# Kernel optimization log

Measured on AMD Instinct MI355X. Metric: run time of the kernel, lower is better.

Reference implementation:

```python
import jax, jax.numpy as jnp
import numpy as np

D_MODEL = 1024
NUM_HEAD = 16
BATCH = 2
SEQ = 2048
NEG_INF = -1e9  # matches masked_fill value in the original


def setup_inputs() -> dict:
    key = jax.random.key(0)
    k1, k2, k3, k4, k5 = jax.random.split(key, 5)
    scale = 1.0 / np.sqrt(D_MODEL)
    return {
        "x": jax.random.normal(k1, (BATCH, SEQ, D_MODEL), dtype=jnp.float32),
        "q_weight": jax.random.normal(k2, (D_MODEL, D_MODEL), dtype=jnp.float32) * scale,
        "k_weight": jax.random.normal(k3, (D_MODEL, D_MODEL), dtype=jnp.float32) * scale,
        "v_weight": jax.random.normal(k4, (D_MODEL, D_MODEL), dtype=jnp.float32) * scale,
        "o_weight": jax.random.normal(k5, (D_MODEL, D_MODEL), dtype=jnp.float32) * scale,
    }


def reference(x, q_weight, k_weight, v_weight, o_weight):
    b, s, d = x.shape
    h = NUM_HEAD
    dh = d // h
    # projections: weight layout is (d_out, d_in)
    q = jnp.einsum('bsd,ed->bse', x, q_weight).reshape(b, s, h, dh).transpose(0, 2, 1, 3)
    k = jnp.einsum('bsd,ed->bse', x, k_weight).reshape(b, s, h, dh).transpose(0, 2, 1, 3)
    v = jnp.einsum('bsd,ed->bse', x, v_weight).reshape(b, s, h, dh).transpose(0, 2, 1, 3)
    scores = jnp.einsum('bhqd,bhkd->bhqk', q, k) / jnp.sqrt(jnp.asarray(dh, x.dtype))
    causal = jnp.triu(jnp.ones((s, s), dtype=bool), k=1)  # True above diagonal -> masked
    scores = jnp.where(causal, jnp.asarray(NEG_INF, x.dtype), scores)
    attn = jax.nn.softmax(scores, axis=-1)
    out = jnp.einsum('bhqk,bhkd->bhqd', attn, v)          # [b,h,s,dh]
    out = out.transpose(0, 2, 1, 3).reshape(b, s, d)       # merge heads
    return jnp.einsum('bse,de->bsd', out, o_weight)
```

## Files before the change

### kernel.cpp

```cpp
#include <hip/hip_runtime.h>

typedef short bhalf8 __attribute__((ext_vector_type(8)));
typedef float floatx4 __attribute__((ext_vector_type(4)));

#define D_MODEL 1024
#define SEQ     2048
#define BATCH   2
#define NHEAD   16
#define DH      64

#define GLDS(g, l) __builtin_amdgcn_global_load_lds( \
    (const __attribute__((address_space(1))) void*)(g), \
    (__attribute__((address_space(3))) void*)(l), 16, 0, 0)

static __device__ __forceinline__ short f2bf(float f) {
    unsigned u = __builtin_bit_cast(unsigned, f);
    u = (u + 0x7fffu + ((u >> 16) & 1u)) >> 16;
    return (short)u;
}
static __device__ __forceinline__ unsigned pack2(float a, float b) {
    return (unsigned)(unsigned short)f2bf(a) | ((unsigned)(unsigned short)f2bf(b) << 16);
}
static __device__ __forceinline__ unsigned cvt_pk_bf16(float lo, float hi) {
    unsigned r;
    asm("v_cvt_pk_bf16_f32 %0, %1, %2" : "=v"(r) : "v"(lo), "v"(hi));
    return r;
}

__global__ __launch_bounds__(256) void cast_x(const float* __restrict__ s,
                                              short* __restrict__ d) {
    int i = (blockIdx.x * 256 + threadIdx.x) * 8;
    float4 a = *(const float4*)(s + i);
    float4 b = *(const float4*)(s + i + 4);
    uint4 u = {pack2(a.x, a.y), pack2(a.z, a.w), pack2(b.x, b.y), pack2(b.z, b.w)};
    *(uint4*)(d + i) = u;
}

__global__ __launch_bounds__(256) void cast_w(const float* __restrict__ wq,
                                              const float* __restrict__ wk,
                                              const float* __restrict__ wv,
                                              const float* __restrict__ wo,
                                              short* __restrict__ dst) {
    const float* s = (blockIdx.y == 0) ? wq : (blockIdx.y == 1) ? wk
                   : (blockIdx.y == 2) ? wv : wo;
    size_t off = (size_t)blockIdx.y * (D_MODEL * D_MODEL);
    int i = (blockIdx.x * 256 + threadIdx.x) * 8;
    float4 a = *(const float4*)(s + i);
    float4 b = *(const float4*)(s + i + 4);
    uint4 u = {pack2(a.x, a.y), pack2(a.z, a.w), pack2(b.x, b.y), pack2(b.z, b.w)};
    *(uint4*)(dst + off + i) = u;
}

__global__ __launch_bounds__(256) void gemm_qkv(const short* __restrict__ A,
                                                const short* __restrict__ W,
                                                short* __restrict__ Qo,
                                                short* __restrict__ Ko,
                                                short* __restrict__ Vt) {
    __shared__ __align__(16) char pool[34816];
    short (*As)[64] = (short(*)[64])pool;
    short (*Bs)[64] = (short(*)[64])(pool + 16384);
    const int t    = threadIdx.x;
    const int wave = t >> 6, lane = t & 63, quad = lane >> 4, l16 = lane & 15;
    const int bm = blockIdx.x * 128, by = blockIdx.y, bn = by * 128;
    const int qm = (wave >> 1) * 64, qn = (wave & 1) * 64;

    const int lrow = lane >> 3, lcol = (lane & 7) * 8;
    const short* Ag = A + (size_t)(bm + wave * 32 + lrow) * 1024 + lcol;
    const short* Wg = W + (size_t)(bn + wave * 32 + lrow) * 1024 + lcol;
    short* Al = &As[wave * 32][0];
    short* Bl = &Bs[wave * 32][0];

    floatx4 acc[4][4];
#pragma unroll
    for (int i = 0; i < 4; ++i)
#pragma unroll
        for (int j = 0; j < 4; ++j) {
            floatx4 z = {0.f, 0.f, 0.f, 0.f};
            acc[i][j] = z;
        }

    for (int k0 = 0; k0 < 1024; k0 += 64) {
        __syncthreads();
#pragma unroll
        for (int j = 0; j < 4; ++j) {
            GLDS(Ag + k0 + (size_t)j * 8 * 1024, Al + j * 8 * 64);
            GLDS(Wg + k0 + (size_t)j * 8 * 1024, Bl + j * 8 * 64);
        }
        __syncthreads();
#pragma unroll
        for (int kk = 0; kk < 64; kk += 32) {
            bhalf8 af[4], bfr[4];
#pragma unroll
            for (int im = 0; im < 4; ++im)
                af[im] = *(const bhalf8*)&As[qm + im * 16 + l16][kk + quad * 8];
#pragma unroll
            for (int jn = 0; jn < 4; ++jn)
                bfr[jn] = *(const bhalf8*)&Bs[qn + jn * 16 + l16][kk + quad * 8];
#pragma unroll
            for (int im = 0; im < 4; ++im)
#pragma unroll
                for (int jn = 0; jn < 4; ++jn)
                    acc[im][jn] = __builtin_amdgcn_mfma_f32_16x16x32_bf16(
                        af[im], bfr[jn], acc[im][jn], 0, 0, 0);
        }
    }

    __syncthreads();
    short (*Ct)[136] = (short(*)[136])pool;
    const bool isV = (by >= 16);
#pragma unroll
    for (int im = 0; im < 4; ++im)
#pragma unroll
        for (int jn = 0; jn < 4; ++jn)
#pragma unroll
            for (int g = 0; g < 4; ++g) {
                const int ml = qm + im * 16 + quad * 4 + g;
                const int nl = qn + jn * 16 + l16;
                if (isV) Ct[nl][ml] = f2bf(acc[im][jn][g]);
                else     Ct[ml][nl] = f2bf(acc[im][jn][g]);
            }
    __syncthreads();

    short* outp;
    size_t rowbase, colbase, stride;
    if (by < 8)       { outp = Qo; rowbase = bm;                colbase = bn;        stride = 1024; }
    else if (by < 16) { outp = Ko; rowbase = bm;                colbase = bn - 1024; stride = 1024; }
    else              { outp = Vt; rowbase = (size_t)bn - 2048; colbase = bm;        stride = 4096; }
#pragma unroll
    for (int pass = 0; pass < 8; ++pass) {
        const int r = (t >> 4) + pass * 16;
        const int c = (t & 15) * 8;
        uint4 u = *(const uint4*)&Ct[r][c];
        *(uint4*)(outp + (rowbase + r) * stride + colbase + c) = u;
    }
}

__global__ __launch_bounds__(256) void gemm_o(const short* __restrict__ A,
                                              const short* __restrict__ W,
                                              float* __restrict__ C) {
    __shared__ __align__(16) char pool[34816];
    short (*As)[64] = (short(*)[64])pool;
    short (*Bs)[64] = (short(*)[64])(pool + 16384);
    const int t    = threadIdx.x;
    const int wave = t >> 6, lane = t & 63, quad = lane >> 4, l16 = lane & 15;
    const int bm = blockIdx.x * 128, bn = blockIdx.y * 64;
    const int qm = (wave >> 1) * 64, qn = (wave & 1) * 32;

    const int lrow = lane >> 3, lcol = (lane & 7) * 8;
    const short* Ag = A + (size_t)(bm + wave * 32 + lrow) * 1024 + lcol;
    const short* Wg = W + (size_t)(bn + wave * 16 + lrow) * 1024 + lcol;
    short* Al = &As[wave * 32][0];
    short* Bl = &Bs[wave * 16][0];

    floatx4 acc[4][2];
#pragma unroll
    for (int i = 0; i < 4; ++i)
#pragma unroll
        for (int j = 0; j < 2; ++j) {
            floatx4 z = {0.f, 0.f, 0.f, 0.f};
            acc[i][j] = z;
        }

    for (int k0 = 0; k0 < 1024; k0 += 64) {
        __syncthreads();
#pragma unroll
        for (int j = 0; j < 4; ++j)
            GLDS(Ag + k0 + (size_t)j * 8 * 1024, Al + j * 8 * 64);
#pragma unroll
        for (int j = 0; j < 2; ++j)
            GLDS(Wg + k0 + (size_t)j * 8 * 1024, Bl + j * 8 * 64);
        __syncthreads();
#pragma unroll
        for (int kk = 0; kk < 64; kk += 32) {
            bhalf8 af[4], bfr[2];
#pragma unroll
            for (int im = 0; im < 4; ++im)
                af[im] = *(const bhalf8*)&As[qm + im * 16 + l16][kk + quad * 8];
#pragma unroll
            for (int jn = 0; jn < 2; ++jn)
                bfr[jn] = *(const bhalf8*)&Bs[qn + jn * 16 + l16][kk + quad * 8];
#pragma unroll
            for (int im = 0; im < 4; ++im)
#pragma unroll
                for (int jn = 0; jn < 2; ++jn)
                    acc[im][jn] = __builtin_amdgcn_mfma_f32_16x16x32_bf16(
                        af[im], bfr[jn], acc[im][jn], 0, 0, 0);
        }
    }

    __syncthreads();
    float (*Ctf)[68] = (float(*)[68])pool;
#pragma unroll
    for (int im = 0; im < 4; ++im)
#pragma unroll
        for (int jn = 0; jn < 2; ++jn)
#pragma unroll
            for (int g = 0; g < 4; ++g)
                Ctf[qm + im * 16 + quad * 4 + g][qn + jn * 16 + l16] = acc[im][jn][g];
    __syncthreads();
#pragma unroll
    for (int pass = 0; pass < 8; ++pass) {
        const int r = (t >> 4) + pass * 16;
        const int c = (t & 15) * 4;
        float4 u = *(const float4*)&Ctf[r][c];
        *(float4*)(C + (size_t)(bm + r) * 1024 + bn + c) = u;
    }
}

#define LOADQ(qf, qwv) do {                                                   \
    _Pragma("unroll")                                                         \
    for (int im_ = 0; im_ < 2; ++im_) {                                       \
        const short* qr_ = Qbase + (size_t)((qwv) + im_ * 16 + l16) * 1024;   \
        qf[im_][0] = *(const bhalf8*)(qr_ + quad * 8);                        \
        qf[im_][1] = *(const bhalf8*)(qr_ + 32 + quad * 8);                   \
    } } while (0)

#define LOADK(dst, kk) do {                                                   \
    _Pragma("unroll")                                                         \
    for (int jn_ = 0; jn_ < 4; ++jn_) {                                       \
        const short* kr_ = Kbase + (size_t)((kk) + jn_ * 16 + l16) * 1024 + quad * 8; \
        dst[jn_][0] = *(const bhalf8*)(kr_);                                  \
        dst[jn_][1] = *(const bhalf8*)(kr_ + 32);                             \
    } } while (0)

#define LOADV(dst, kk) do {                                                   \
    _Pragma("unroll")                                                         \
    for (int nd_ = 0; nd_ < 4; ++nd_) {                                       \
        const short* vr_ = Vbase + (size_t)(nd_ * 16 + l16) * 4096 + (kk) + quad * 8; \
        dst[nd_][0] = *(const bhalf8*)(vr_);                                  \
        dst[nd_][1] = *(const bhalf8*)(vr_ + 32);                             \
    } } while (0)

#define ZERO_ACC() do {                                                       \
    _Pragma("unroll")                                                         \
    for (int im_ = 0; im_ < 2; ++im_) {                                       \
        _Pragma("unroll")                                                     \
        for (int g_ = 0; g_ < 4; ++g_) lsum[im_][g_] = 0.f;                   \
        _Pragma("unroll")                                                     \
        for (int nd_ = 0; nd_ < 4; ++nd_) {                                   \
            floatx4 z_ = {0.f, 0.f, 0.f, 0.f};                                \
            o[im_][nd_] = z_;                                                 \
        }                                                                     \
    } } while (0)

#define CHUNK(k0v, knv, qf, qwv) do {                                         \
    floatx4 s_[2][4];                                                         \
    _Pragma("unroll")                                                         \
    for (int im_ = 0; im_ < 2; ++im_)                                         \
        _Pragma("unroll")                                                     \
        for (int jn_ = 0; jn_ < 4; ++jn_) {                                   \
            floatx4 z_ = {0.f, 0.f, 0.f, 0.f};                                \
            z_ = __builtin_amdgcn_mfma_f32_16x16x32_bf16(qf[im_][0], kf[jn_][0], z_, 0, 0, 0); \
            z_ = __builtin_amdgcn_mfma_f32_16x16x32_bf16(qf[im_][1], kf[jn_][1], z_, 0, 0, 0); \
            s_[im_][jn_] = z_;                                                \
        }                                                                     \
    LOADK(kf, knv);                                \
    const bool partial_ = ((k0v) + 64 > (qwv));                               \
    _Pragma("unroll")                                                         \
    for (int im_ = 0; im_ < 2; ++im_)                                         \
        _Pragma("unroll")                                                     \
        for (int g_ = 0; g_ < 4; ++g_) {                                      \
            const int rr_ = im_ * 16 + quad * 4 + g_;                         \
            const int qrow_ = (qwv) + rr_;                                    \
            float e0_ = exp2f(s_[im_][0][g_] * KS - CB);                      \
            float e1_ = exp2f(s_[im_][1][g_] * KS - CB);                      \
            float e2_ = exp2f(s_[im_][2][g_] * KS - CB);                      \
            float e3_ = exp2f(s_[im_][3][g_] * KS - CB);                      \
            if (partial_) {                                                   \
                if ((k0v) + l16 > qrow_)      e0_ = 0.f;                      \
                if ((k0v) + 16 + l16 > qrow_) e1_ = 0.f;                      \
                if ((k0v) + 32 + l16 > qrow_) e2_ = 0.f;                      \
                if ((k0v) + 48 + l16 > qrow_) e3_ = 0.f;                      \
            }                                                                 \
            lsum[im_][g_] += (e0_ + e1_) + (e2_ + e3_);                       \
            unsigned r01_ = cvt_pk_bf16(e0_, e1_);                            \
            unsigned r23_ = cvt_pk_bf16(e2_, e3_);                            \
            Ps[wave][rr_][l16]      = (short)r01_;                            \
            Ps[wave][rr_][16 + l16] = (short)(r01_ >> 16);                    \
            Ps[wave][rr_][32 + l16] = (short)r23_;                            \
            Ps[wave][rr_][48 + l16] = (short)(r23_ >> 16);                    \
        }                                                                     \
    _Pragma("unroll")                                                         \
    for (int im_ = 0; im_ < 2; ++im_) {                                       \
        bhalf8 ap0_ = *(const bhalf8*)&Ps[wave][im_ * 16 + l16][quad * 8];    \
        bhalf8 ap1_ = *(const bhalf8*)&Ps[wave][im_ * 16 + l16][32 + quad * 8]; \
        _Pragma("unroll")                                                     \
        for (int nd_ = 0; nd_ < 4; ++nd_) {                                   \
            o[im_][nd_] = __builtin_amdgcn_mfma_f32_16x16x32_bf16(ap0_, vt[nd_][0], o[im_][nd_], 0, 0, 0); \
            o[im_][nd_] = __builtin_amdgcn_mfma_f32_16x16x32_bf16(ap1_, vt[nd_][1], o[im_][nd_], 0, 0, 0); \
        }                                                                     \
    }                                                                         \
    LOADV(vt, knv);                                     \
} while (0)

#define RUN_SEG(nseg, kbase, qf, qwv) do {                                    \
    const int n_ = (nseg);                                                    \
    const int base_ = (kbase);                                                \
    if (n_ > 0) {                                                             \
        LOADK(kf, base_);                                                     \
        LOADV(vt, base_);                                                     \
        _Pragma("unroll 1")                                                   \
        for (int i_ = 0; i_ < n_; ++i_) {                                     \
            const int k0_ = base_ + i_ * 64;                                  \
            const int kn_ = (i_ + 1 < n_) ? (k0_ + 64) : base_;               \
            CHUNK(k0_, kn_, qf, qwv);                                         \
        }                                                                     \
    } } while (0)

#define REDUCE_LSUM() do {                                                    \
    _Pragma("unroll")                                                         \
    for (int im_ = 0; im_ < 2; ++im_)                                         \
        _Pragma("unroll")                                                     \
        for (int g_ = 0; g_ < 4; ++g_) {                                      \
            float r_ = lsum[im_][g_];                                         \
            r_ += __shfl_xor(r_, 1, 64);                                      \
            r_ += __shfl_xor(r_, 2, 64);                                      \
            r_ += __shfl_xor(r_, 4, 64);                                      \
            r_ += __shfl_xor(r_, 8, 64);                                      \
            lsum[im_][g_] = r_;                                               \
        } } while (0)

#define STORE_OUT(qwv) do {                                                   \
    _Pragma("unroll")                                                         \
    for (int im_ = 0; im_ < 2; ++im_)                                         \
        _Pragma("unroll")                                                     \
        for (int g_ = 0; g_ < 4; ++g_) {                                      \
            const float iv_ = 1.0f / lsum[im_][g_];                           \
            const int qrow_ = (qwv) + im_ * 16 + quad * 4 + g_;               \
            _Pragma("unroll")                                                 \
            for (int nd_ = 0; nd_ < 4; ++nd_)                                 \
                Y[(size_t)(b * SEQ + qrow_) * 1024 + h * 64 + nd_ * 16 + l16] = \
                    f2bf(o[im_][nd_][g_] * iv_);                              \
        } } while (0)

__global__ __launch_bounds__(512) void attn_v8(const short* __restrict__ Qo,
                                               const short* __restrict__ Ko,
                                               const short* __restrict__ Vt,
                                               short* __restrict__ Y) {
    __shared__ __align__(16) char pool[45056];
    short (*Ps)[32][72] = (short(*)[32][72])pool;
    float (*Cmb)[44]    = (float(*)[44])pool;

    const int t    = threadIdx.x;
    const int wave = t >> 6, lane = t & 63, quad = lane >> 4, l16 = lane & 15;
    const int bh = blockIdx.x, b = bh >> 4, h = bh & 15;
    const bool isA = (wave < 4);
    const int j   = (int)blockIdx.y * 4 + (wave & 3);
    const int sH  = 63 - j;
    const int qwH = sH * 32, qwL = j * 32;
    const int ncH = (65 - j) >> 1;
    const int ncL = (j + 2) >> 1;

    const short* Qbase = Qo + (size_t)b * SEQ * 1024 + h * 64;
    const short* Kbase = Ko + (size_t)b * SEQ * 1024 + h * 64;
    const short* Vbase = Vt + (size_t)h * 64 * 4096 + (size_t)b * SEQ;

    const float KS = 0.125f * 1.44269504f;
    const float CB = 12.0f * 1.44269504f;

    bhalf8 kf[4][2], vt[4][2];
    float lsum[2][4];
    floatx4 o[2][4];
    ZERO_ACC();

    if (isA) {
        bhalf8 qfH[2][2];
        LOADQ(qfH, qwH);
        RUN_SEG(17, 0, qfH, qwH);
        REDUCE_LSUM();
    } else {
        {
            bhalf8 qfL[2][2];
            LOADQ(qfL, qwL);
            RUN_SEG(ncL, 0, qfL, qwL);
            REDUCE_LSUM();
            STORE_OUT(qwL);
        }
        ZERO_ACC();
        {
            bhalf8 qfH[2][2];
            LOADQ(qfH, qwH);
            RUN_SEG(ncH - 17, 1088, qfH, qwH);
            REDUCE_LSUM();
        }
    }

    __syncthreads();
    if (!isA) {
        float* cp = &Cmb[(wave - 4) * 64 + lane][0];
#pragma unroll
        for (int im = 0; im < 2; ++im)
#pragma unroll
            for (int nd = 0; nd < 4; ++nd)
                *(floatx4*)(cp + (im * 4 + nd) * 4) = o[im][nd];
#pragma unroll
        for (int im = 0; im < 2; ++im)
#pragma unroll
            for (int g = 0; g < 4; ++g)
                cp[32 + im * 4 + g] = lsum[im][g];
    }
    __syncthreads();
    if (isA) {
        const float* cp = &Cmb[wave * 64 + lane][0];
#pragma unroll
        for (int im = 0; im < 2; ++im)
#pragma unroll
            for (int nd = 0; nd < 4; ++nd) {
                floatx4 add = *(const floatx4*)(cp + (im * 4 + nd) * 4);
                o[im][nd] += add;
            }
#pragma unroll
        for (int im = 0; im < 2; ++im)
#pragma unroll
            for (int g = 0; g < 4; ++g)
                lsum[im][g] += cp[32 + im * 4 + g];
        STORE_OUT(qwH);
    }
}

extern "C" void kernel_launch(void* const* d_in, const int* in_sizes, int n_in,
                              void* d_out, int out_size, void* d_ws, size_t ws_size,
                              hipStream_t stream) {
    const float* x  = (const float*)d_in[0];
    const float* wq = (const float*)d_in[1];
    const float* wk = (const float*)d_in[2];
    const float* wv = (const float*)d_in[3];
    const float* wo = (const float*)d_in[4];

    short* xb   = (short*)d_ws;
    short* Qo   = xb + (size_t)4096 * 1024;
    short* Ko   = Qo + (size_t)4096 * 1024;
    short* Vt   = Ko + (size_t)4096 * 1024;
    short* wall = Vt + (size_t)1024 * 4096;
    short* wob  = wall + (size_t)3 * 1024 * 1024;

    cast_x<<<dim3(2048), 256, 0, stream>>>(x, xb);
    cast_w<<<dim3(512, 4), 256, 0, stream>>>(wq, wk, wv, wo, wall);
    gemm_qkv<<<dim3(32, 24), 256, 0, stream>>>(xb, wall, Qo, Ko, Vt);
    attn_v8<<<dim3(BATCH * NHEAD, 8), 512, 0, stream>>>(Qo, Ko, Vt, xb);
    gemm_o<<<dim3(32, 16), 256, 0, stream>>>(xb, wob, (float*)d_out);
}
```

Before: 221.9 us.

## Split attention work per query pair across four waves with interleaved key chunks

Each 256-thread block now handles one low/high query-tile pair, with four waves splitting the key range by interleaving 64-key chunks at a stride of 128. Partial accumulators and row sums are combined through shared-memory slots in several synchronised stages. This gives a finer grid (32 blocks per head instead of 8) and smaller blocks, aiming at better load balance and occupancy. The cost is extra shared-memory reductions and barriers, plus reloading the Q fragments per wave.

Result: slower. 326.0 us (+46.9%).

```diff
diff --git a/kernel.cpp b/kernel.cpp
--- a/kernel.cpp
+++ b/kernel.cpp
@@ -293,7 +293,7 @@
     LOADV(vt, knv);                                     \
 } while (0)
 
-#define RUN_SEG(nseg, kbase, qf, qwv) do {                                    \
+#define RUN_SEG(nseg, kbase, kstep, qf, qwv) do {                             \
     const int n_ = (nseg);                                                    \
     const int base_ = (kbase);                                                \
     if (n_ > 0) {                                                             \
@@ -301,8 +301,8 @@
         LOADV(vt, base_);                                                     \
         _Pragma("unroll 1")                                                   \
         for (int i_ = 0; i_ < n_; ++i_) {                                     \
-            const int k0_ = base_ + i_ * 64;                                  \
-            const int kn_ = (i_ + 1 < n_) ? (k0_ + 64) : base_;               \
+            const int k0_ = base_ + i_ * (kstep);                             \
+            const int kn_ = (i_ + 1 < n_) ? (k0_ + (kstep)) : base_;          \
             CHUNK(k0_, kn_, qf, qwv);                                         \
         }                                                                     \
     } } while (0)
@@ -320,6 +320,34 @@
             lsum[im_][g_] = r_;                                               \
         } } while (0)
 
+#define WRITE_PART(slot_) do {                                                \
+    float* cp_ = (float*)(slot_) + lane * 40;                                 \
+    _Pragma("unroll")                                                         \
+    for (int im_ = 0; im_ < 2; ++im_)                                         \
+        _Pragma("unroll")                                                     \
+        for (int nd_ = 0; nd_ < 4; ++nd_)                                     \
+            *(floatx4*)(cp_ + (im_ * 4 + nd_) * 4) = o[im_][nd_];             \
+    _Pragma("unroll")                                                         \
+    for (int im_ = 0; im_ < 2; ++im_)                                         \
+        _Pragma("unroll")                                                     \
+        for (int g_ = 0; g_ < 4; ++g_)                                        \
+            cp_[32 + im_ * 4 + g_] = lsum[im_][g_];                           \
+    } while (0)
+
+#define ACCUM_PART(slot_) do {                                                \
+    const float* cp_ = (const float*)(slot_) + lane * 40;                     \
+    _Pragma("unroll")                                                         \
+    for (int im_ = 0; im_ < 2; ++im_)                                         \
+        _Pragma("unroll")                                                     \
+        for (int nd_ = 0; nd_ < 4; ++nd_)                                     \
+            o[im_][nd_] += *(const floatx4*)(cp_ + (im_ * 4 + nd_) * 4);      \
+    _Pragma("unroll")                                                         \
+    for (int im_ = 0; im_ < 2; ++im_)                                         \
+        _Pragma("unroll")                                                     \
+        for (int g_ = 0; g_ < 4; ++g_)                                        \
+            lsum[im_][g_] += cp_[32 + im_ * 4 + g_];                          \
+    } while (0)
+
 #define STORE_OUT(qwv) do {                                                   \
     _Pragma("unroll")                                                         \
     for (int im_ = 0; im_ < 2; ++im_)                                         \
@@ -333,23 +361,23 @@
                     f2bf(o[im_][nd_][g_] * iv_);                              \
         } } while (0)
 
-__global__ __launch_bounds__(512) void attn_v8(const short* __restrict__ Qo,
-                                               const short* __restrict__ Ko,
-                                               const short* __restrict__ Vt,
-                                               short* __restrict__ Y) {
-    __shared__ __align__(16) char pool[45056];
+__global__ __launch_bounds__(256, 4) void attn_v9(const short* __restrict__ Qo,
+                                                  const short* __restrict__ Ko,
+                                                  const short* __restrict__ Vt,
+                                                  short* __restrict__ Y) {
+    __shared__ __align__(16) char pool[38912];
     short (*Ps)[32][72] = (short(*)[32][72])pool;
-    float (*Cmb)[44]    = (float(*)[44])pool;
+    float* PsR  = (float*)pool;
+    float* Cmb0 = (float*)(pool + 18432);
+    float* Cmb1 = (float*)(pool + 18432 + 10240);
 
     const int t    = threadIdx.x;
     const int wave = t >> 6, lane = t & 63, quad = lane >> 4, l16 = lane & 15;
     const int bh = blockIdx.x, b = bh >> 4, h = bh & 15;
-    const bool isA = (wave < 4);
-    const int j   = (int)blockIdx.y * 4 + (wave & 3);
-    const int sH  = 63 - j;
-    const int qwH = sH * 32, qwL = j * 32;
-    const int ncH = (65 - j) >> 1;
-    const int ncL = (j + 2) >> 1;
+    const int j = (int)blockIdx.y;
+    const int qwH = (63 - j) * 32, qwL = j * 32;
+    const int ncL  = (j + 2) >> 1;
+    const int tail = ((65 - j) >> 1) - 17;
 
     const short* Qbase = Qo + (size_t)b * SEQ * 1024 + h * 64;
     const short* Kbase = Ko + (size_t)b * SEQ * 1024 + h * 64;
@@ -363,57 +391,66 @@
     floatx4 o[2][4];
     ZERO_ACC();
 
-    if (isA) {
-        bhalf8 qfH[2][2];
-        LOADQ(qfH, qwH);
-        RUN_SEG(17, 0, qfH, qwH);
+    if (wave == 0) {
+        bhalf8 qf[2][2];
+        LOADQ(qf, qwH);
+        RUN_SEG(9, 0, 128, qf, qwH);
         REDUCE_LSUM();
+    } else if (wave == 1) {
+        bhalf8 qf[2][2];
+        LOADQ(qf, qwH);
+        RUN_SEG(8, 64, 128, qf, qwH);
+        REDUCE_LSUM();
+    } else if (wave == 2) {
+        {
+            bhalf8 qf[2][2];
+            LOADQ(qf, qwL);
+            RUN_SEG((ncL + 1) >> 1, 0, 128, qf, qwL);
+            REDUCE_LSUM();
+        }
+        WRITE_PART(Cmb0);
+        ZERO_ACC();
+        {
+            bhalf8 qf[2][2];
+            LOADQ(qf, qwH);
+            RUN_SEG((tail + 1) >> 1, 1088, 128, qf, qwH);
+            REDUCE_LSUM();
+        }
     } else {
         {
-            bhalf8 qfL[2][2];
-            LOADQ(qfL, qwL);
-            RUN_SEG(ncL, 0, qfL, qwL);
+            bhalf8 qf[2][2];
+            LOADQ(qf, qwL);
+            RUN_SEG(ncL >> 1, 64, 128, qf, qwL);
             REDUCE_LSUM();
-            STORE_OUT(qwL);
-        }
+        }
+        WRITE_PART(Cmb1);
         ZERO_ACC();
         {
-            bhalf8 qfH[2][2];
-            LOADQ(qfH, qwH);
-            RUN_SEG(ncH - 17, 1088, qfH, qwH);
+            bhalf8 qf[2][2];
+            LOADQ(qf, qwH);
+            RUN_SEG(tail >> 1, 1152, 128, qf, qwH);
             REDUCE_LSUM();
         }
     }
 
     __syncthreads();
-    if (!isA) {
-        float* cp = &Cmb[(wave - 4) * 64 + lane][0];
-#pragma unroll
-        for (int im = 0; im < 2; ++im)
-#pragma unroll
-            for (int nd = 0; nd < 4; ++nd)
-                *(floatx4*)(cp + (im * 4 + nd) * 4) = o[im][nd];
-#pragma unroll
-        for (int im = 0; im < 2; ++im)
-#pragma unroll
-            for (int g = 0; g < 4; ++g)
-                cp[32 + im * 4 + g] = lsum[im][g];
-    }
-    __syncthreads();
-    if (isA) {
-        const float* cp = &Cmb[wave * 64 + lane][0];
-#pragma unroll
-        for (int im = 0; im < 2; ++im)
-#pragma unroll
-            for (int nd = 0; nd < 4; ++nd) {
-                floatx4 add = *(const floatx4*)(cp + (im * 4 + nd) * 4);
-                o[im][nd] += add;
-            }
-#pragma unroll
-        for (int im = 0; im < 2; ++im)
-#pragma unroll
-            for (int g = 0; g < 4; ++g)
-                lsum[im][g] += cp[32 + im * 4 + g];
+    if (wave == 1) WRITE_PART(PsR);
+    __syncthreads();
+    if (wave == 0) {
+        ACCUM_PART(PsR);
+    } else if (wave == 1) {
+        ZERO_ACC();
+        ACCUM_PART(Cmb0);
+        ACCUM_PART(Cmb1);
+        STORE_OUT(qwL);
+    }
+    __syncthreads();
+    if (wave == 2)      WRITE_PART(Cmb0);
+    else if (wave == 3) WRITE_PART(Cmb1);
+    __syncthreads();
+    if (wave == 0) {
+        ACCUM_PART(Cmb0);
+        ACCUM_PART(Cmb1);
         STORE_OUT(qwH);
     }
 }
@@ -437,6 +474,6 @@
     cast_x<<<dim3(2048), 256, 0, stream>>>(x, xb);
     cast_w<<<dim3(512, 4), 256, 0, stream>>>(wq, wk, wv, wo, wall);
     gemm_qkv<<<dim3(32, 24), 256, 0, stream>>>(xb, wall, Qo, Ko, Vt);
-    attn_v8<<<dim3(BATCH * NHEAD, 8), 512, 0, stream>>>(Qo, Ko, Vt, xb);
+    attn_v9<<<dim3(BATCH * NHEAD, 32), 256, 0, stream>>>(Qo, Ko, Vt, xb);
     gemm_o<<<dim3(32, 16), 256, 0, stream>>>(xb, wob, (float*)d_out);
 }
```
